# Optimization experiments

Measured on AMD Instinct MI355X. Metric: run time of the kernel, lower is better.

Reference implementation:

```python
import jax, jax.numpy as jnp
import numpy as np

N_NODES = 100000


def sage_conv(x, src, dst, w_self, w_neigh, b):
    # DGL SAGEConv with 'mean' aggregator: out = x @ W_self + mean_neigh(x) @ W_neigh + b
    msg = x[src]                                                     # [E, d] gather
    agg = jax.ops.segment_sum(msg, dst, num_segments=N_NODES)        # [N, d]
    deg = jax.ops.segment_sum(jnp.ones((src.shape[0],), x.dtype), dst,
                              num_segments=N_NODES)                  # [N]
    h_neigh = agg / jnp.maximum(deg, 1.0)[:, None]                   # mean; 0 for isolated nodes
    return x @ w_self + h_neigh @ w_neigh + b


def setup_inputs() -> dict:
    key = jax.random.key(0)
    ks = jax.random.split(key, 12)
    N, E = N_NODES, 1600000
    in_f, h_f, r_f = 128, 128, 64
    glorot = lambda k, i, o: jax.random.normal(k, (i, o), jnp.float32) / np.float32(np.sqrt(i))
    return {
        "in_feat": jax.random.normal(ks[0], (N, in_f), jnp.float32),
        "src": jax.random.randint(ks[1], (E,), 0, N),
        "dst": jax.random.randint(ks[2], (E,), 0, N),
        "w1_self": glorot(ks[3], in_f, h_f), "w1_neigh": glorot(ks[4], in_f, h_f), "b1": jnp.zeros((h_f,), jnp.float32),
        "w2_self": glorot(ks[5], h_f, r_f), "w2_neigh": glorot(ks[6], h_f, r_f), "b2": jnp.zeros((r_f,), jnp.float32),
        "w3_self": glorot(ks[7], r_f, r_f), "w3_neigh": glorot(ks[8], r_f, r_f), "b3": jnp.zeros((r_f,), jnp.float32),
    }


def reference(in_feat, src, dst,
              w1_self, w1_neigh, b1,
              w2_self, w2_neigh, b2,
              w3_self, w3_neigh, b3):
    h = sage_conv(in_feat, src, dst, w1_self, w1_neigh, b1)
    h = jax.nn.relu(h)
    h = sage_conv(h, src, dst, w2_self, w2_neigh, b2)
    h = jax.nn.relu(h)
    # dropout is treated as identity (deterministic eval-mode reference)
    h = sage_conv(h, src, dst, w3_self, w3_neigh, b3)
    return jax.nn.softmax(h, axis=-1)
```

## Files before the change

### kernel.cpp

```cpp
#include <hip/hip_runtime.h>
#include <hip/hip_bf16.h>

#define N_NODES 100000

typedef unsigned short ushort_t;
typedef __attribute__((ext_vector_type(8))) short short8;
typedef __attribute__((ext_vector_type(4))) float f32x4;

static __device__ __forceinline__ ushort_t f2bf(float f) {
    unsigned u = __float_as_uint(f);
    unsigned r = u + 0x7FFFu + ((u >> 16) & 1u);
    return (ushort_t)(r >> 16);
}
static __device__ __forceinline__ float bf2f(ushort_t h) {
    return __uint_as_float(((unsigned)h) << 16);
}

static __device__ __forceinline__ void split8(const float* __restrict__ xp,
                                              short8& hi, short8& lo) {
    float4 x0 = *(const float4*)xp;
    float4 x1 = *(const float4*)(xp + 4);
    float xs[8] = {x0.x, x0.y, x0.z, x0.w, x1.x, x1.y, x1.z, x1.w};
    #pragma unroll
    for (int j = 0; j < 8; ++j) {
        ushort_t h = f2bf(xs[j]);
        hi[j] = (short)h;
        lo[j] = (short)f2bf(xs[j] - bf2f(h));
    }
}

__global__ __launch_bounds__(256) void hist_kernel(const int* __restrict__ dst,
                                                   int* __restrict__ deg, int E) {
    int e = blockIdx.x * 256 + threadIdx.x;
    if (e < E) atomicAdd(&deg[__builtin_nontemporal_load(&dst[e])], 1);
}

__global__ __launch_bounds__(256) void scan_partial_sums(const int* __restrict__ deg,
                                                         int* __restrict__ partials, int N) {
    __shared__ int wsums[4];
    int tid = threadIdx.x, lane = tid & 63, wv = tid >> 6;
    int i0 = blockIdx.x * 1024 + tid * 4;
    int s = 0;
    #pragma unroll
    for (int j = 0; j < 4; ++j) {
        int i = i0 + j;
        if (i < N) s += deg[i];
    }
    #pragma unroll
    for (int off = 32; off > 0; off >>= 1) s += __shfl_xor(s, off, 64);
    if (lane == 0) wsums[wv] = s;
    __syncthreads();
    if (tid == 0)
        partials[blockIdx.x] = wsums[0] + wsums[1] + wsums[2] + wsums[3];
}

__global__ __launch_bounds__(256) void scan_partials(int* __restrict__ partials, int NB,
                                                     int* __restrict__ row_ptr, int N) {
    __shared__ int wsums[4];
    int tid = threadIdx.x, lane = tid & 63, wv = tid >> 6;
    int v = (tid < NB) ? partials[tid] : 0;
    int x = v;
    #pragma unroll
    for (int off = 1; off < 64; off <<= 1) {
        int y = __shfl_up(x, off, 64);
        if (lane >= off) x += y;
    }
    if (lane == 63) wsums[wv] = x;
    __syncthreads();
    int woff = 0;
    for (int w = 0; w < wv; ++w) woff += wsums[w];
    int incl = x + woff;
    if (tid < NB) partials[tid] = incl - v;
    if (tid == NB - 1) row_ptr[N] = incl;
}

__global__ __launch_bounds__(256) void scan_emit(const int* __restrict__ deg,
                                                 const int* __restrict__ partials,
                                                 int* __restrict__ row_ptr,
                                                 int* __restrict__ cursor,
                                                 float* __restrict__ inv_deg, int N) {
    __shared__ int wsums[4];
    int tid = threadIdx.x, lane = tid & 63, wv = tid >> 6;
    int i0 = blockIdx.x * 1024 + tid * 4;
    int d[4];
    #pragma unroll
    for (int j = 0; j < 4; ++j) {
        int i = i0 + j;
        d[j] = (i < N) ? deg[i] : 0;
    }
    int s = d[0] + d[1] + d[2] + d[3];
    int x = s;
    #pragma unroll
    for (int off = 1; off < 64; off <<= 1) {
        int y = __shfl_up(x, off, 64);
        if (lane >= off) x += y;
    }
    if (lane == 63) wsums[wv] = x;
    __syncthreads();
    int woff = 0;
    for (int w = 0; w < wv; ++w) woff += wsums[w];
    int run = partials[blockIdx.x] + woff + x - s;
    #pragma unroll
    for (int j = 0; j < 4; ++j) {
        int i = i0 + j;
        if (i < N) {
            row_ptr[i] = run;
            cursor[i]  = run;
            inv_deg[i] = 1.0f / (float)(d[j] > 0 ? d[j] : 1);
            run += d[j];
        }
    }
}

#define FILL_GROUPS 8
#define FILL_BPG    128
__global__ __launch_bounds__(256) void fill_part(const int* __restrict__ src,
                                                 const int* __restrict__ dst,
                                                 int* __restrict__ cursor,
                                                 int* __restrict__ edge_src,
                                                 int E, int N) {
    int g    = blockIdx.x & (FILL_GROUPS - 1);
    int bInG = blockIdx.x >> 3;
    int lo = (int)((long long)N * g / FILL_GROUPS);
    int hi = (int)((long long)N * (g + 1) / FILL_GROUPS);
    int stride = FILL_BPG * 256;
    for (int e = bInG * 256 + threadIdx.x; e < E; e += stride) {
        int d = __builtin_nontemporal_load(&dst[e]);
        if (d >= lo && d < hi) {
            int sv = __builtin_nontemporal_load(&src[e]);
            int p = atomicAdd(&cursor[d], 1);
            edge_src[p] = sv;
        }
    }
}

__global__ __launch_bounds__(256) void pack_all(
        const float* __restrict__ W0, const float* __restrict__ W1,
        const float* __restrict__ W2, const float* __restrict__ W3,
        const float* __restrict__ W4, const float* __restrict__ W5,
        ushort_t* H0, ushort_t* L0, ushort_t* H1, ushort_t* L1,
        ushort_t* H2, ushort_t* L2, ushort_t* H3, ushort_t* L3,
        ushort_t* H4, ushort_t* L4, ushort_t* H5, ushort_t* L5) {
    int b = blockIdx.x;
    const float* W; ushort_t* Hi; ushort_t* Lo; int K, NS, base;
    if (b < 8)       { W = W0; Hi = H0; Lo = L0; K = 128; NS = 128; base = 0;  }
    else if (b < 16) { W = W1; Hi = H1; Lo = L1; K = 128; NS = 128; base = 8;  }
    else if (b < 20) { W = W2; Hi = H2; Lo = L2; K = 128; NS = 64;  base = 16; }
    else if (b < 24) { W = W3; Hi = H3; Lo = L3; K = 128; NS = 64;  base = 20; }
    else if (b < 26) { W = W4; Hi = H4; Lo = L4; K = 64;  NS = 64;  base = 24; }
    else             { W = W5; Hi = H5; Lo = L5; K = 64;  NS = 64;  base = 26; }
    int tid = (b - base) * 256 + threadIdx.x;
    if (tid >= (K * NS) / 8) return;
    int l  = tid & 63;
    int fl = tid >> 6;
    int NT = NS / 16;
    int t = fl % NT, s = fl / NT;
    ushort_t hs[8], ls[8];
    #pragma unroll
    for (int j = 0; j < 8; ++j) {
        int k = s * 32 + (l >> 4) * 8 + j;
        int n = t * 16 + (l & 15);
        float w = W[(size_t)k * NS + n];
        ushort_t h = f2bf(w);
        hs[j] = h;
        ls[j] = f2bf(w - bf2f(h));
    }
    #pragma unroll
    for (int j = 0; j < 8; ++j) {
        Hi[(size_t)tid * 8 + j] = hs[j];
        Lo[(size_t)tid * 8 + j] = ls[j];
    }
}

template <int K, int NS>
__global__ __launch_bounds__(256) void mfma_gemm(const float* __restrict__ X,
                                                 const ushort_t* __restrict__ BsHi,
                                                 const ushort_t* __restrict__ BsLo,
                                                 const ushort_t* __restrict__ BnHi,
                                                 const ushort_t* __restrict__ BnLo,
                                                 const float* __restrict__ bias,
                                                 float* __restrict__ S,
                                                 ushort_t* __restrict__ Zb,
                                                 int M) {
    constexpr int KS = K / 32;
    constexpr int NT = NS / 16;
    int tid = threadIdx.x;
    int lane = tid & 63, w = tid >> 6;
    int baseM = blockIdx.x * 128 + w * 32;
    int rIn = lane & 15, q = lane >> 4;

    short8 Ahi[KS][2], Alo[KS][2];
    #pragma unroll
    for (int s = 0; s < KS; ++s) {
        #pragma unroll
        for (int mt = 0; mt < 2; ++mt) {
            int gm = baseM + mt * 16 + rIn;
            if (gm < M) {
                split8(&X[(size_t)gm * K + s * 32 + q * 8], Ahi[s][mt], Alo[s][mt]);
            } else {
                #pragma unroll
                for (int j = 0; j < 8; ++j) { Ahi[s][mt][j] = 0; Alo[s][mt][j] = 0; }
            }
        }
    }

    for (int t = 0; t < NT; ++t) {
        f32x4 aS0 = {0.f, 0.f, 0.f, 0.f}, aS1 = {0.f, 0.f, 0.f, 0.f};
        f32x4 aZ0 = {0.f, 0.f, 0.f, 0.f}, aZ1 = {0.f, 0.f, 0.f, 0.f};
        #pragma unroll
        for (int s = 0; s < KS; ++s) {
            size_t fo = ((size_t)(s * NT + t) * 64 + lane) * 8;
            short8 bsh = *(const short8*)&BsHi[fo];
            short8 bsl = *(const short8*)&BsLo[fo];
            short8 bnh = *(const short8*)&BnHi[fo];
            short8 bnl = *(const short8*)&BnLo[fo];
            aS0 = __builtin_amdgcn_mfma_f32_16x16x32_bf16(Ahi[s][0], bsh, aS0, 0, 0, 0);
            aS0 = __builtin_amdgcn_mfma_f32_16x16x32_bf16(Alo[s][0], bsh, aS0, 0, 0, 0);
            aS0 = __builtin_amdgcn_mfma_f32_16x16x32_bf16(Ahi[s][0], bsl, aS0, 0, 0, 0);
            aS1 = __builtin_amdgcn_mfma_f32_16x16x32_bf16(Ahi[s][1], bsh, aS1, 0, 0, 0);
            aS1 = __builtin_amdgcn_mfma_f32_16x16x32_bf16(Alo[s][1], bsh, aS1, 0, 0, 0);
            aS1 = __builtin_amdgcn_mfma_f32_16x16x32_bf16(Ahi[s][1], bsl, aS1, 0, 0, 0);
            aZ0 = __builtin_amdgcn_mfma_f32_16x16x32_bf16(Ahi[s][0], bnh, aZ0, 0, 0, 0);
            aZ0 = __builtin_amdgcn_mfma_f32_16x16x32_bf16(Alo[s][0], bnh, aZ0, 0, 0, 0);
            aZ0 = __builtin_amdgcn_mfma_f32_16x16x32_bf16(Ahi[s][0], bnl, aZ0, 0, 0, 0);
            aZ1 = __builtin_amdgcn_mfma_f32_16x16x32_bf16(Ahi[s][1], bnh, aZ1, 0, 0, 0);
            aZ1 = __builtin_amdgcn_mfma_f32_16x16x32_bf16(Alo[s][1], bnh, aZ1, 0, 0, 0);
            aZ1 = __builtin_amdgcn_mfma_f32_16x16x32_bf16(Ahi[s][1], bnl, aZ1, 0, 0, 0);
        }
        int col = t * 16 + rIn;
        float bv = bias[col];
        #pragma unroll
        for (int mt = 0; mt < 2; ++mt) {
            f32x4 aS = mt ? aS1 : aS0;
            f32x4 aZ = mt ? aZ1 : aZ0;
            #pragma unroll
            for (int r = 0; r < 4; ++r) {
                int gm = baseM + mt * 16 + q * 4 + r;
                if (gm < M) {
                    S[(size_t)gm * NS + col]  = aS[r] + bv;
                    Zb[(size_t)gm * NS + col] = f2bf(aZ[r]);
                }
            }
        }
    }
}

template <int D, int ACT>
__global__ __launch_bounds__(256) void agg_kernel(const float* __restrict__ S,
                                                  const uint2* __restrict__ Zu,
                                                  const int* __restrict__ row_ptr,
                                                  const int* __restrict__ edge_src,
                                                  const float* __restrict__ inv_deg,
                                                  float* __restrict__ out, int N) {
    constexpr int G  = D / 4;
    constexpr int NG = 256 / G;
    int tid = threadIdx.x;
    int g = tid / G, f4 = tid % G;
    int n = blockIdx.x * NG + g;
    if (n >= N) return;
    int beg = row_ptr[n], end = row_ptr[n + 1];

    float a0[4] = {0, 0, 0, 0}, a1[4] = {0, 0, 0, 0};
    float a2[4] = {0, 0, 0, 0}, a3[4] = {0, 0, 0, 0};
#define ACC(u, a)                                                              \
    a[0] += __uint_as_float((u).x << 16);                                      \
    a[1] += __uint_as_float((u).x & 0xFFFF0000u);                              \
    a[2] += __uint_as_float((u).y << 16);                                      \
    a[3] += __uint_as_float((u).y & 0xFFFF0000u);
    int j = beg;
    for (; j + 3 < end; j += 4) {
        int s0 = edge_src[j + 0], s1 = edge_src[j + 1];
        int s2 = edge_src[j + 2], s3 = edge_src[j + 3];
        uint2 u0 = Zu[(size_t)s0 * G + f4];
        uint2 u1 = Zu[(size_t)s1 * G + f4];
        uint2 u2 = Zu[(size_t)s2 * G + f4];
        uint2 u3 = Zu[(size_t)s3 * G + f4];
        ACC(u0, a0) ACC(u1, a1) ACC(u2, a2) ACC(u3, a3)
    }
    for (; j < end; ++j) {
        uint2 u = Zu[(size_t)edge_src[j] * G + f4];
        ACC(u, a0)
    }
#undef ACC
    float id = inv_deg[n];
    float4 sv = ((const float4*)(S + (size_t)n * D))[f4];
    float v[4];
    v[0] = sv.x + id * ((a0[0] + a1[0]) + (a2[0] + a3[0]));
    v[1] = sv.y + id * ((a0[1] + a1[1]) + (a2[1] + a3[1]));
    v[2] = sv.z + id * ((a0[2] + a1[2]) + (a2[2] + a3[2]));
    v[3] = sv.w + id * ((a0[3] + a1[3]) + (a2[3] + a3[3]));

    float4 o;
    if (ACT == 0) {
        o.x = fmaxf(v[0], 0.f); o.y = fmaxf(v[1], 0.f);
        o.z = fmaxf(v[2], 0.f); o.w = fmaxf(v[3], 0.f);
    } else {
        float m = fmaxf(fmaxf(v[0], v[1]), fmaxf(v[2], v[3]));
        #pragma unroll
        for (int off = 8; off > 0; off >>= 1) m = fmaxf(m, __shfl_xor(m, off, 16));
        float e0 = __expf(v[0] - m), e1 = __expf(v[1] - m);
        float e2 = __expf(v[2] - m), e3 = __expf(v[3] - m);
        float s = (e0 + e1) + (e2 + e3);
        #pragma unroll
        for (int off = 8; off > 0; off >>= 1) s += __shfl_xor(s, off, 16);
        float inv = 1.0f / s;
        o.x = e0 * inv; o.y = e1 * inv; o.z = e2 * inv; o.w = e3 * inv;
    }
    ((float4*)(out + (size_t)n * D))[f4] = o;
}

extern "C" void kernel_launch(void* const* d_in, const int* in_sizes, int n_in,
                              void* d_out, int out_size, void* d_ws, size_t ws_size,
                              hipStream_t stream) {
    const float* in_feat = (const float*)d_in[0];
    const int*   src     = (const int*)d_in[1];
    const int*   dst     = (const int*)d_in[2];
    const float* w1s = (const float*)d_in[3];
    const float* w1n = (const float*)d_in[4];
    const float* b1  = (const float*)d_in[5];
    const float* w2s = (const float*)d_in[6];
    const float* w2n = (const float*)d_in[7];
    const float* b2  = (const float*)d_in[8];
    const float* w3s = (const float*)d_in[9];
    const float* w3n = (const float*)d_in[10];
    const float* b3  = (const float*)d_in[11];

    const int N = N_NODES;
    const int E = in_sizes[1];

    char* p = (char*)d_ws;
    auto carve = [&](size_t bytes) -> char* {
        char* q = p;
        p += (bytes + 511) & ~(size_t)511;
        return q;
    };
    float*    S        = (float*)   carve((size_t)N * 128 * sizeof(float));
    ushort_t* Zb       = (ushort_t*)carve((size_t)N * 128 * sizeof(ushort_t));
    float*    H        = (float*)   carve((size_t)N * 128 * sizeof(float));
    int*      edge_src = (int*)     carve((size_t)E * sizeof(int));
    int*      row_ptr  = (int*)     carve((size_t)(N + 1) * sizeof(int));
    int*      cursor   = (int*)     carve((size_t)N * sizeof(int));
    int*      deg      = (int*)     carve((size_t)N * sizeof(int));
    float*    invd     = (float*)   carve((size_t)N * sizeof(float));
    int*      partials = (int*)     carve(256 * sizeof(int));
    ushort_t* P1sH = (ushort_t*)carve(128 * 128 * 2); ushort_t* P1sL = (ushort_t*)carve(128 * 128 * 2);
    ushort_t* P1nH = (ushort_t*)carve(128 * 128 * 2); ushort_t* P1nL = (ushort_t*)carve(128 * 128 * 2);
    ushort_t* P2sH = (ushort_t*)carve(128 * 64 * 2);  ushort_t* P2sL = (ushort_t*)carve(128 * 64 * 2);
    ushort_t* P2nH = (ushort_t*)carve(128 * 64 * 2);  ushort_t* P2nL = (ushort_t*)carve(128 * 64 * 2);
    ushort_t* P3sH = (ushort_t*)carve(64 * 64 * 2);   ushort_t* P3sL = (ushort_t*)carve(64 * 64 * 2);
    ushort_t* P3nH = (ushort_t*)carve(64 * 64 * 2);   ushort_t* P3nL = (ushort_t*)carve(64 * 64 * 2);

    pack_all<<<28, 256, 0, stream>>>(w1s, w1n, w2s, w2n, w3s, w3n,
                                     P1sH, P1sL, P1nH, P1nL,
                                     P2sH, P2sL, P2nH, P2nL,
                                     P3sH, P3sL, P3nH, P3nL);

    hipMemsetAsync(deg, 0, (size_t)N * sizeof(int), stream);
    hist_kernel<<<(E + 255) / 256, 256, 0, stream>>>(dst, deg, E);
    const int NB = (N + 1023) / 1024;
    scan_partial_sums<<<NB, 256, 0, stream>>>(deg, partials, N);
    scan_partials<<<1, 256, 0, stream>>>(partials, NB, row_ptr, N);
    scan_emit<<<NB, 256, 0, stream>>>(deg, partials, row_ptr, cursor, invd, N);
    fill_part<<<FILL_GROUPS * FILL_BPG, 256, 0, stream>>>(src, dst, cursor, edge_src, E, N);

    const int GB = (N + 127) / 128;

    mfma_gemm<128, 128><<<GB, 256, 0, stream>>>(in_feat, P1sH, P1sL, P1nH, P1nL, b1, S, Zb, N);
    agg_kernel<128, 0><<<(N + 7) / 8, 256, 0, stream>>>(S, (const uint2*)Zb,
                                                        row_ptr, edge_src, invd, H, N);

    mfma_gemm<128, 64><<<GB, 256, 0, stream>>>(H, P2sH, P2sL, P2nH, P2nL, b2, S, Zb, N);
    agg_kernel<64, 0><<<(N + 15) / 16, 256, 0, stream>>>(S, (const uint2*)Zb,
                                                         row_ptr, edge_src, invd, H, N);

    mfma_gemm<64, 64><<<GB, 256, 0, stream>>>(H, P3sH, P3sL, P3nH, P3nL, b3, S, Zb, N);
    agg_kernel<64, 1><<<(N + 15) / 16, 256, 0, stream>>>(S, (const uint2*)Zb,
                                                         row_ptr, edge_src, invd,
                                                         (float*)d_out, N);
}
```

Before: 517.4 us.

## Replace partitioned CSR fill with two-pass bucketed binning and per-bucket scatter

The old CSR fill pass made 8 groups of blocks each read the whole edge list and keep only the edges whose destination fell in their range, so dst was read eight times. The new code splits this into two passes. First, each block counts its chunk of edges into 256-node buckets in shared memory, reserves space per bucket with one global atomic, and writes (dst,src) pairs into a staging buffer that reuses the H workspace. Second, one block per bucket scatters those pairs into the CSR edge list using per-node cursor atomics, now confined to a small, cache-local node range. The cost is an extra pass over 8-byte pairs, and the result depends on H being free until the first aggregation.

```diff
diff --git a/kernel.cpp b/kernel.cpp
--- a/kernel.cpp
+++ b/kernel.cpp
@@ -78,7 +78,8 @@
                                                  const int* __restrict__ partials,
                                                  int* __restrict__ row_ptr,
                                                  int* __restrict__ cursor,
-                                                 float* __restrict__ inv_deg, int N) {
+                                                 float* __restrict__ inv_deg,
+                                                 int* __restrict__ gcur, int N) {
     __shared__ int wsums[4];
     int tid = threadIdx.x, lane = tid & 63, wv = tid >> 6;
     int i0 = blockIdx.x * 1024 + tid * 4;
@@ -107,30 +108,58 @@
             row_ptr[i] = run;
             cursor[i]  = run;
             inv_deg[i] = 1.0f / (float)(d[j] > 0 ? d[j] : 1);
+            if ((i & 255) == 0) gcur[i >> 8] = run;
             run += d[j];
         }
     }
 }
 
-#define FILL_GROUPS 8
-#define FILL_BPG    128
-__global__ __launch_bounds__(256) void fill_part(const int* __restrict__ src,
+#define MAXBUCK 512
+__global__ __launch_bounds__(256) void bin_pairs(const int* __restrict__ src,
                                                  const int* __restrict__ dst,
-                                                 int* __restrict__ cursor,
-                                                 int* __restrict__ edge_src,
-                                                 int E, int N) {
-    int g    = blockIdx.x & (FILL_GROUPS - 1);
-    int bInG = blockIdx.x >> 3;
-    int lo = (int)((long long)N * g / FILL_GROUPS);
-    int hi = (int)((long long)N * (g + 1) / FILL_GROUPS);
-    int stride = FILL_BPG * 256;
-    for (int e = bInG * 256 + threadIdx.x; e < E; e += stride) {
+                                                 int* __restrict__ gcur,
+                                                 long long* __restrict__ staged,
+                                                 int E, int NBUCK, int C) {
+    __shared__ int cnt[MAXBUCK];
+    int tid = threadIdx.x;
+    int e0 = blockIdx.x * C;
+    int e1 = min(e0 + C, E);
+    for (int b = tid; b < NBUCK; b += 256) cnt[b] = 0;
+    __syncthreads();
+    for (int e = e0 + tid; e < e1; e += 256) {
         int d = __builtin_nontemporal_load(&dst[e]);
-        if (d >= lo && d < hi) {
-            int sv = __builtin_nontemporal_load(&src[e]);
-            int p = atomicAdd(&cursor[d], 1);
-            edge_src[p] = sv;
-        }
+        atomicAdd(&cnt[d >> 8], 1);
+    }
+    __syncthreads();
+    for (int b = tid; b < NBUCK; b += 256) {
+        int c = cnt[b];
+        cnt[b] = (c > 0) ? atomicAdd(&gcur[b], c) : 0;
+    }
+    __syncthreads();
+    for (int e = e0 + tid; e < e1; e += 256) {
+        int d = __builtin_nontemporal_load(&dst[e]);
+        int s = __builtin_nontemporal_load(&src[e]);
+        int p = atomicAdd(&cnt[d >> 8], 1);
+        staged[p] = ((long long)d << 32) | (unsigned)s;
+    }
+}
+
+__global__ __launch_bounds__(256) void scatter_bucket(const long long* __restrict__ staged,
+                                                      const int* __restrict__ row_ptr,
+                                                      int* __restrict__ cursor,
+                                                      int* __restrict__ edge_src,
+                                                      int N) {
+    int b = blockIdx.x;
+    int lo = b << 8;
+    int hiN = min((b + 1) << 8, N);
+    int gstart = row_ptr[lo];
+    int gend   = row_ptr[hiN];
+    for (int p = gstart + threadIdx.x; p < gend; p += 256) {
+        long long pr = __builtin_nontemporal_load(&staged[p]);
+        int d = (int)(pr >> 32);
+        int s = (int)(pr & 0xFFFFFFFFll);
+        int pos = atomicAdd(&cursor[d], 1);
+        edge_src[pos] = s;
     }
 }
 
@@ -343,6 +372,8 @@
     int*      deg      = (int*)     carve((size_t)N * sizeof(int));
     float*    invd     = (float*)   carve((size_t)N * sizeof(float));
     int*      partials = (int*)     carve(256 * sizeof(int));
+    int*      gcur     = (int*)     carve(MAXBUCK * sizeof(int));
+    long long* staged  = (long long*)H;
     ushort_t* P1sH = (ushort_t*)carve(128 * 128 * 2); ushort_t* P1sL = (ushort_t*)carve(128 * 128 * 2);
     ushort_t* P1nH = (ushort_t*)carve(128 * 128 * 2); ushort_t* P1nL = (ushort_t*)carve(128 * 128 * 2);
     ushort_t* P2sH = (ushort_t*)carve(128 * 64 * 2);  ushort_t* P2sL = (ushort_t*)carve(128 * 64 * 2);
@@ -355,13 +386,17 @@
                                      P2sH, P2sL, P2nH, P2nL,
                                      P3sH, P3sL, P3nH, P3nL);
 
-    hipMemsetAsync(deg, 0, (size_t)N * sizeof(int), stream);
+    (void)hipMemsetAsync(deg, 0, (size_t)N * sizeof(int), stream);
     hist_kernel<<<(E + 255) / 256, 256, 0, stream>>>(dst, deg, E);
     const int NB = (N + 1023) / 1024;
     scan_partial_sums<<<NB, 256, 0, stream>>>(deg, partials, N);
     scan_partials<<<1, 256, 0, stream>>>(partials, NB, row_ptr, N);
-    scan_emit<<<NB, 256, 0, stream>>>(deg, partials, row_ptr, cursor, invd, N);
-    fill_part<<<FILL_GROUPS * FILL_BPG, 256, 0, stream>>>(src, dst, cursor, edge_src, E, N);
+    scan_emit<<<NB, 256, 0, stream>>>(deg, partials, row_ptr, cursor, invd, gcur, N);
+    const int NBUCK = (N + 255) >> 8;
+    const int BINB  = 256;
+    const int CHUNK = (E + BINB - 1) / BINB;
+    bin_pairs<<<BINB, 256, 0, stream>>>(src, dst, gcur, staged, E, NBUCK, CHUNK);
+    scatter_bucket<<<NBUCK, 256, 0, stream>>>(staged, row_ptr, cursor, edge_src, N);
 
     const int GB = (N + 127) / 128;
 
```

Result: faster. 504.8 us (-2.4%).
